# Kernel optimization log

Hardware: AMD Instinct MI355X
Metric: run time of the kernel (lower is better)

## Reference

```python
import jax, jax.numpy as jnp
import numpy as np
import math

NUM_BUCKETS = 32
MAX_DISTANCE = 128
NUM_HEADS = 16
D_MODEL = 1024
HEAD_DIM = D_MODEL // NUM_HEADS


def _relative_position_bucket(relative_position, num_buckets=NUM_BUCKETS, max_distance=MAX_DISTANCE):
    # bidirectional=False path of the original
    rp = -jnp.minimum(relative_position, 0)  # non-negative distances
    max_exact = num_buckets // 2
    is_small = rp < max_exact
    rp_safe = jnp.maximum(rp, 1).astype(jnp.float32)
    rp_if_large = max_exact + (
        jnp.log(rp_safe / max_exact) / math.log(max_distance / max_exact) * (num_buckets - max_exact)
    ).astype(jnp.int32)
    rp_if_large = jnp.minimum(rp_if_large, num_buckets - 1)
    return jnp.where(is_small, rp, rp_if_large)


def relative_bias(rab_weight, q_len, k_len):
    ctx = jnp.arange(q_len)[:, None]
    mem = jnp.arange(k_len)[None, :]
    buckets = _relative_position_bucket(mem - ctx)  # [Q, K]
    vals = rab_weight[buckets]                       # [Q, K, H]
    return jnp.transpose(vals, (2, 0, 1))[None]      # [1, H, Q, K]


def setup_inputs() -> dict:
    key = jax.random.key(0)
    k1, k2, k3, k4 = jax.random.split(key, 4)
    B, S = 4, 2048
    return {
        "v": jax.random.normal(k1, (B, S, D_MODEL), dtype=jnp.float32),
        "k": jax.random.normal(k2, (B, S, D_MODEL), dtype=jnp.float32),
        "q": jax.random.normal(k3, (B, S, D_MODEL), dtype=jnp.float32),
        "rab_weight": jax.random.normal(k4, (NUM_BUCKETS, NUM_HEADS), dtype=jnp.float32),
    }


def reference(v, k, q, rab_weight):
    B, S, _ = q.shape
    def split(x):
        return jnp.transpose(x.reshape(B, S, NUM_HEADS, HEAD_DIM), (0, 2, 1, 3))  # [B,H,S,D]
    qh, kh, vh = split(q), split(k), split(v)
    scores = jnp.einsum("bhqd,bhkd->bhqk", qh, kh)          # [B,H,S,S]
    scores = scores + relative_bias(rab_weight, S, S)        # add relative bias
    av = jnp.einsum("bhqk,bhkd->bhqd", jax.nn.silu(scores), vh)
    return jnp.transpose(av, (0, 2, 1, 3)).reshape(B, S, D_MODEL)
```

## Files before the change

### kernel.cpp

```cpp
#include <hip/hip_runtime.h>

#define NB 4
#define SEQ 2048
#define NH 16
#define HD 64
#define DMODEL 1024

typedef short bf16x8 __attribute__((ext_vector_type(8)));
typedef float f32x16 __attribute__((ext_vector_type(16)));

union FragU {
    bf16x8 v;
    uint2 u2[2];
    unsigned int w[4];
    unsigned short s[8];
};

#if __has_builtin(__builtin_amdgcn_cvt_pk_bf16_f32)
typedef __bf16 v2bf_t __attribute__((ext_vector_type(2)));
__device__ __forceinline__ unsigned int pack_bf16(float lo, float hi) {
    union { v2bf_t h; unsigned int u; } cv;
    cv.h = __builtin_amdgcn_cvt_pk_bf16_f32(lo, hi);
    return cv.u;
}
#else
__device__ __forceinline__ unsigned int pack_bf16(float lo, float hi) {
    unsigned int a = __float_as_uint(lo) + 0x8000u;
    unsigned int b = __float_as_uint(hi) + 0x8000u;
    return __builtin_amdgcn_perm(b, a, 0x07060302);
}
#endif

#define EXP_SCALE 1.44269504f
#define LN2       0.69314718f

__global__ __launch_bounds__(256, 2)
void paa_kernel(const float* __restrict__ Vg, const float* __restrict__ Kg,
                const float* __restrict__ Qg, const float* __restrict__ RW,
                float* __restrict__ Og)
{
    __shared__ __align__(16) unsigned short KsLds[64 * 68];
    __shared__ __align__(16) unsigned short VtLds[64 * 68];
    __shared__ float btab[128];

    const int tid  = threadIdx.x;
    const int lane = tid & 63;
    const int wave = tid >> 6;
    const int half = lane >> 5;
    const int l31  = lane & 31;

    const int bid  = blockIdx.x;
    const int bh   = bid & 63;
    const int qt   = bid >> 6;
    const int b    = bh >> 4;
    const int head = bh & 15;

    const int q0w = qt * 256 + wave * 64;

    if (tid < 128) {
        int rp = tid;
        int bucket;
        if (rp < 16) bucket = rp;
        else {
            int big = 16 + (int)(logf((float)rp * 0.0625f) * 7.6943736f);
            bucket = big < 31 ? big : 31;
        }
        btab[tid] = RW[bucket * NH + head] * EXP_SCALE;
    }

    FragU qf[2][4];
    {
        const float* qbase = Qg + (size_t)(b * SEQ) * DMODEL + head * HD;
        #pragma unroll
        for (int u = 0; u < 2; ++u) {
            const float* qrow = qbase + (size_t)(q0w + u * 32 + l31) * DMODEL;
            #pragma unroll
            for (int kf = 0; kf < 4; ++kf) {
                int dd = kf * 16 + half * 8;
                float4 x0 = *(const float4*)(qrow + dd);
                float4 x1 = *(const float4*)(qrow + dd + 4);
                FragU f;
                f.w[0] = pack_bf16(x0.x * EXP_SCALE, x0.y * EXP_SCALE);
                f.w[1] = pack_bf16(x0.z * EXP_SCALE, x0.w * EXP_SCALE);
                f.w[2] = pack_bf16(x1.x * EXP_SCALE, x1.y * EXP_SCALE);
                f.w[3] = pack_bf16(x1.z * EXP_SCALE, x1.w * EXP_SCALE);
                qf[u][kf] = f;
            }
        }
    }

    f32x16 oacc[2][2];
    #pragma unroll
    for (int u = 0; u < 2; ++u)
        #pragma unroll
        for (int n = 0; n < 2; ++n)
            #pragma unroll
            for (int r = 0; r < 16; ++r) oacc[u][n][r] = 0.0f;

    __syncthreads();
    const float bias_d0  = btab[0];
    const float bias_far = btab[127];

    const int krow0 = tid >> 4;
    const int c4    = tid & 15;
    const int kc4   = tid >> 4;
    const int d4    = tid & 15;

    const float* kthr = Kg + (size_t)(b * SEQ) * DMODEL + head * HD
                      + (size_t)krow0 * DMODEL + c4 * 4;
    const float* vthr = Vg + (size_t)(b * SEQ) * DMODEL + head * HD
                      + (size_t)(kc4 * 4) * DMODEL + d4 * 4;

    float4 kreg[4], vreg[4];
    #pragma unroll
    for (int i = 0; i < 4; ++i) kreg[i] = *(const float4*)(kthr + (size_t)(i * 16) * DMODEL);
    #pragma unroll
    for (int r = 0; r < 4; ++r) vreg[r] = *(const float4*)(vthr + (size_t)r * DMODEL);

    for (int it = 0; it < 32; ++it) {
        const int kcb = it * 64;

        #pragma unroll
        for (int i = 0; i < 4; ++i) {
            uint2 w;
            w.x = pack_bf16(kreg[i].x, kreg[i].y);
            w.y = pack_bf16(kreg[i].z, kreg[i].w);
            *(uint2*)&KsLds[(krow0 + i * 16) * 68 + c4 * 4] = w;
        }
        {
            const float* vr = (const float*)vreg;
            #pragma unroll
            for (int c = 0; c < 4; ++c) {
                uint2 w;
                w.x = pack_bf16(vr[0 * 4 + c], vr[1 * 4 + c]);
                w.y = pack_bf16(vr[2 * 4 + c], vr[3 * 4 + c]);
                *(uint2*)&VtLds[(d4 * 4 + c) * 68 + kc4 * 4] = w;
            }
        }
        __syncthreads();

        if (it < 31) {
            const float* kn = kthr + (size_t)(kcb + 64) * DMODEL;
            const float* vn = vthr + (size_t)(kcb + 64) * DMODEL;
            #pragma unroll
            for (int i = 0; i < 4; ++i) kreg[i] = *(const float4*)(kn + (size_t)(i * 16) * DMODEL);
            #pragma unroll
            for (int r = 0; r < 4; ++r) vreg[r] = *(const float4*)(vn + (size_t)r * DMODEL);
        }

        FragU pf[2][4];
        #pragma unroll
        for (int t = 0; t < 2; ++t) {
            const int kcmin = kcb + t * 32;
            FragU ka[4];
            #pragma unroll
            for (int kf = 0; kf < 4; ++kf) {
                int off = (t * 32 + l31) * 68 + kf * 16 + half * 8;
                ka[kf].u2[0] = *(const uint2*)&KsLds[off];
                ka[kf].u2[1] = *(const uint2*)&KsLds[off + 4];
            }
            f32x16 st[2];
            #pragma unroll
            for (int u = 0; u < 2; ++u) {
                const int qminu = q0w + u * 32;
                if (qminu + 31 - kcmin <= 0) {
                    #pragma unroll
                    for (int r = 0; r < 16; ++r) st[u][r] = bias_d0;
                } else if (qminu - (kcmin + 31) >= 113) {
                    #pragma unroll
                    for (int r = 0; r < 16; ++r) st[u][r] = bias_far;
                } else {
                    const int dql = qminu + l31 - kcmin - 4 * half;
                    #pragma unroll
                    for (int r = 0; r < 16; ++r) {
                        int dv = dql - ((r & 3) + 8 * (r >> 2));
                        dv = dv < 0 ? 0 : (dv > 127 ? 127 : dv);
                        st[u][r] = btab[dv];
                    }
                }
            }
            #pragma unroll
            for (int kf = 0; kf < 4; ++kf)
                #pragma unroll
                for (int u = 0; u < 2; ++u)
                    st[u] = __builtin_amdgcn_mfma_f32_32x32x16_bf16(
                        ka[kf].v, qf[u][kf].v, st[u], 0, 0, 0);

            #pragma unroll
            for (int u = 0; u < 2; ++u) {
                float vals[16];
                #pragma unroll
                for (int r = 0; r < 16; ++r) {
                    float x = st[u][r];
                    float e = __builtin_amdgcn_exp2f(-x);
                    vals[r] = x * __builtin_amdgcn_rcpf(1.0f + e);
                }
                #pragma unroll
                for (int j = 0; j < 4; ++j)
                    pf[u][t * 2].w[j]     = pack_bf16(vals[2 * j], vals[2 * j + 1]);
                #pragma unroll
                for (int j = 0; j < 4; ++j)
                    pf[u][t * 2 + 1].w[j] = pack_bf16(vals[8 + 2 * j], vals[9 + 2 * j]);
            }
        }

        #pragma unroll
        for (int f = 0; f < 4; ++f) {
            #pragma unroll
            for (int n = 0; n < 2; ++n) {
                FragU vf;
                int off = (n * 32 + l31) * 68 + f * 16 + half * 4;
                vf.u2[0] = *(const uint2*)&VtLds[off];
                vf.u2[1] = *(const uint2*)&VtLds[off + 8];
                #pragma unroll
                for (int u = 0; u < 2; ++u)
                    oacc[u][n] = __builtin_amdgcn_mfma_f32_32x32x16_bf16(
                        pf[u][f].v, vf.v, oacc[u][n], 0, 0, 0);
            }
        }
        __syncthreads();
    }

    float* obase = Og + (size_t)(b * SEQ) * DMODEL + head * HD;
    #pragma unroll
    for (int u = 0; u < 2; ++u) {
        #pragma unroll
        for (int r = 0; r < 16; ++r) {
            int q = q0w + u * 32 + (r & 3) + 8 * (r >> 2) + 4 * half;
            float* orow = obase + (size_t)q * DMODEL;
            #pragma unroll
            for (int n = 0; n < 2; ++n)
                orow[n * 32 + l31] = oacc[u][n][r] * LN2;
        }
    }
}

extern "C" void kernel_launch(void* const* d_in, const int* in_sizes, int n_in,
                              void* d_out, int out_size, void* d_ws, size_t ws_size,
                              hipStream_t stream) {
    const float* v  = (const float*)d_in[0];
    const float* k  = (const float*)d_in[1];
    const float* q  = (const float*)d_in[2];
    const float* rw = (const float*)d_in[3];
    float* out = (float*)d_out;
    paa_kernel<<<dim3(512), dim3(256), 0, stream>>>(v, k, q, rw, out);
}
```

Before: 252.5 us.

## Use 512-thread blocks with 32 query rows per wave, dropping register prefetch

Blocks grow from 4 to 8 waves. Each wave now owns 32 query rows instead of 64, so Q fragments, score tiles and output accumulators are halved per thread. The software register prefetch of the next K/V tile is removed: tiles are now loaded from global memory right before being converted and written to LDS. The intent is to cut register pressure and hide memory latency through more resident waves instead of explicit prefetch. In exchange, each wave reads K and V fragments from LDS for half as many MFMAs, and the global loads are no longer overlapped with compute inside a wave.

```diff
diff --git a/kernel.cpp b/kernel.cpp
--- a/kernel.cpp
+++ b/kernel.cpp
@@ -34,7 +34,7 @@
 #define EXP_SCALE 1.44269504f
 #define LN2       0.69314718f
 
-__global__ __launch_bounds__(256, 2)
+__global__ __launch_bounds__(512, 4)
 void paa_kernel(const float* __restrict__ Vg, const float* __restrict__ Kg,
                 const float* __restrict__ Qg, const float* __restrict__ RW,
                 float* __restrict__ Og)
@@ -55,7 +55,7 @@
     const int b    = bh >> 4;
     const int head = bh & 15;
 
-    const int q0w = qt * 256 + wave * 64;
+    const int q0w = qt * 256 + wave * 32;
 
     if (tid < 128) {
         int rp = tid;
@@ -68,87 +68,65 @@
         btab[tid] = RW[bucket * NH + head] * EXP_SCALE;
     }
 
-    FragU qf[2][4];
+    FragU qf[4];
     {
-        const float* qbase = Qg + (size_t)(b * SEQ) * DMODEL + head * HD;
-        #pragma unroll
-        for (int u = 0; u < 2; ++u) {
-            const float* qrow = qbase + (size_t)(q0w + u * 32 + l31) * DMODEL;
-            #pragma unroll
-            for (int kf = 0; kf < 4; ++kf) {
-                int dd = kf * 16 + half * 8;
-                float4 x0 = *(const float4*)(qrow + dd);
-                float4 x1 = *(const float4*)(qrow + dd + 4);
-                FragU f;
-                f.w[0] = pack_bf16(x0.x * EXP_SCALE, x0.y * EXP_SCALE);
-                f.w[1] = pack_bf16(x0.z * EXP_SCALE, x0.w * EXP_SCALE);
-                f.w[2] = pack_bf16(x1.x * EXP_SCALE, x1.y * EXP_SCALE);
-                f.w[3] = pack_bf16(x1.z * EXP_SCALE, x1.w * EXP_SCALE);
-                qf[u][kf] = f;
-            }
-        }
-    }
-
-    f32x16 oacc[2][2];
+        const float* qrow = Qg + (size_t)(b * SEQ + q0w + l31) * DMODEL + head * HD;
+        #pragma unroll
+        for (int kf = 0; kf < 4; ++kf) {
+            int dd = kf * 16 + half * 8;
+            float4 x0 = *(const float4*)(qrow + dd);
+            float4 x1 = *(const float4*)(qrow + dd + 4);
+            FragU f;
+            f.w[0] = pack_bf16(x0.x * EXP_SCALE, x0.y * EXP_SCALE);
+            f.w[1] = pack_bf16(x0.z * EXP_SCALE, x0.w * EXP_SCALE);
+            f.w[2] = pack_bf16(x1.x * EXP_SCALE, x1.y * EXP_SCALE);
+            f.w[3] = pack_bf16(x1.z * EXP_SCALE, x1.w * EXP_SCALE);
+            qf[kf] = f;
+        }
+    }
+
+    f32x16 oacc[2];
     #pragma unroll
-    for (int u = 0; u < 2; ++u)
-        #pragma unroll
-        for (int n = 0; n < 2; ++n)
-            #pragma unroll
-            for (int r = 0; r < 16; ++r) oacc[u][n][r] = 0.0f;
+    for (int n = 0; n < 2; ++n)
+        #pragma unroll
+        for (int r = 0; r < 16; ++r) oacc[n][r] = 0.0f;
 
     __syncthreads();
     const float bias_d0  = btab[0];
     const float bias_far = btab[127];
 
-    const int krow0 = tid >> 4;
-    const int c4    = tid & 15;
-    const int kc4   = tid >> 4;
-    const int d4    = tid & 15;
-
-    const float* kthr = Kg + (size_t)(b * SEQ) * DMODEL + head * HD
-                      + (size_t)krow0 * DMODEL + c4 * 4;
-    const float* vthr = Vg + (size_t)(b * SEQ) * DMODEL + head * HD
-                      + (size_t)(kc4 * 4) * DMODEL + d4 * 4;
-
-    float4 kreg[4], vreg[4];
-    #pragma unroll
-    for (int i = 0; i < 4; ++i) kreg[i] = *(const float4*)(kthr + (size_t)(i * 16) * DMODEL);
-    #pragma unroll
-    for (int r = 0; r < 4; ++r) vreg[r] = *(const float4*)(vthr + (size_t)r * DMODEL);
+    const int krow = tid >> 4;
+    const int c4   = tid & 15;
+    const int kc2  = tid >> 4;
+    const int d4   = tid & 15;
+
+    const float* kbase = Kg + (size_t)(b * SEQ) * DMODEL + head * HD;
+    const float* vbase = Vg + (size_t)(b * SEQ) * DMODEL + head * HD;
 
     for (int it = 0; it < 32; ++it) {
         const int kcb = it * 64;
 
         #pragma unroll
-        for (int i = 0; i < 4; ++i) {
+        for (int i = 0; i < 2; ++i) {
+            int row = krow + i * 32;
+            float4 x = *(const float4*)(kbase + (size_t)(kcb + row) * DMODEL + c4 * 4);
             uint2 w;
-            w.x = pack_bf16(kreg[i].x, kreg[i].y);
-            w.y = pack_bf16(kreg[i].z, kreg[i].w);
-            *(uint2*)&KsLds[(krow0 + i * 16) * 68 + c4 * 4] = w;
+            w.x = pack_bf16(x.x, x.y);
+            w.y = pack_bf16(x.z, x.w);
+            *(uint2*)&KsLds[row * 68 + c4 * 4] = w;
         }
         {
-            const float* vr = (const float*)vreg;
-            #pragma unroll
-            for (int c = 0; c < 4; ++c) {
-                uint2 w;
-                w.x = pack_bf16(vr[0 * 4 + c], vr[1 * 4 + c]);
-                w.y = pack_bf16(vr[2 * 4 + c], vr[3 * 4 + c]);
-                *(uint2*)&VtLds[(d4 * 4 + c) * 68 + kc4 * 4] = w;
-            }
+            const float* vrow = vbase + (size_t)(kcb + kc2 * 2) * DMODEL + d4 * 4;
+            float4 x0 = *(const float4*)(vrow);
+            float4 x1 = *(const float4*)(vrow + DMODEL);
+            *(unsigned int*)&VtLds[(d4 * 4 + 0) * 68 + kc2 * 2] = pack_bf16(x0.x, x1.x);
+            *(unsigned int*)&VtLds[(d4 * 4 + 1) * 68 + kc2 * 2] = pack_bf16(x0.y, x1.y);
+            *(unsigned int*)&VtLds[(d4 * 4 + 2) * 68 + kc2 * 2] = pack_bf16(x0.z, x1.z);
+            *(unsigned int*)&VtLds[(d4 * 4 + 3) * 68 + kc2 * 2] = pack_bf16(x0.w, x1.w);
         }
         __syncthreads();
 
-        if (it < 31) {
-            const float* kn = kthr + (size_t)(kcb + 64) * DMODEL;
-            const float* vn = vthr + (size_t)(kcb + 64) * DMODEL;
-            #pragma unroll
-            for (int i = 0; i < 4; ++i) kreg[i] = *(const float4*)(kn + (size_t)(i * 16) * DMODEL);
-            #pragma unroll
-            for (int r = 0; r < 4; ++r) vreg[r] = *(const float4*)(vn + (size_t)r * DMODEL);
-        }
-
-        FragU pf[2][4];
+        FragU pf[4];
         #pragma unroll
         for (int t = 0; t < 2; ++t) {
             const int kcmin = kcb + t * 32;
@@ -159,49 +137,39 @@
                 ka[kf].u2[0] = *(const uint2*)&KsLds[off];
                 ka[kf].u2[1] = *(const uint2*)&KsLds[off + 4];
             }
-            f32x16 st[2];
-            #pragma unroll
-            for (int u = 0; u < 2; ++u) {
-                const int qminu = q0w + u * 32;
-                if (qminu + 31 - kcmin <= 0) {
-                    #pragma unroll
-                    for (int r = 0; r < 16; ++r) st[u][r] = bias_d0;
-                } else if (qminu - (kcmin + 31) >= 113) {
-                    #pragma unroll
-                    for (int r = 0; r < 16; ++r) st[u][r] = bias_far;
-                } else {
-                    const int dql = qminu + l31 - kcmin - 4 * half;
-                    #pragma unroll
-                    for (int r = 0; r < 16; ++r) {
-                        int dv = dql - ((r & 3) + 8 * (r >> 2));
-                        dv = dv < 0 ? 0 : (dv > 127 ? 127 : dv);
-                        st[u][r] = btab[dv];
-                    }
-                }
-            }
-            #pragma unroll
-            for (int kf = 0; kf < 4; ++kf)
+            f32x16 st;
+            if (q0w + 31 - kcmin <= 0) {
                 #pragma unroll
-                for (int u = 0; u < 2; ++u)
-                    st[u] = __builtin_amdgcn_mfma_f32_32x32x16_bf16(
-                        ka[kf].v, qf[u][kf].v, st[u], 0, 0, 0);
-
-            #pragma unroll
-            for (int u = 0; u < 2; ++u) {
-                float vals[16];
+                for (int r = 0; r < 16; ++r) st[r] = bias_d0;
+            } else if (q0w - (kcmin + 31) >= 113) {
+                #pragma unroll
+                for (int r = 0; r < 16; ++r) st[r] = bias_far;
+            } else {
+                const int dql = q0w + l31 - kcmin - 4 * half;
                 #pragma unroll
                 for (int r = 0; r < 16; ++r) {
-                    float x = st[u][r];
-                    float e = __builtin_amdgcn_exp2f(-x);
-                    vals[r] = x * __builtin_amdgcn_rcpf(1.0f + e);
+                    int dv = dql - ((r & 3) + 8 * (r >> 2));
+                    dv = dv < 0 ? 0 : (dv > 127 ? 127 : dv);
+                    st[r] = btab[dv];
                 }
-                #pragma unroll
-                for (int j = 0; j < 4; ++j)
-                    pf[u][t * 2].w[j]     = pack_bf16(vals[2 * j], vals[2 * j + 1]);
-                #pragma unroll
-                for (int j = 0; j < 4; ++j)
-                    pf[u][t * 2 + 1].w[j] = pack_bf16(vals[8 + 2 * j], vals[9 + 2 * j]);
-            }
+            }
+            #pragma unroll
+            for (int kf = 0; kf < 4; ++kf)
+                st = __builtin_amdgcn_mfma_f32_32x32x16_bf16(ka[kf].v, qf[kf].v, st, 0, 0, 0);
+
+            float vals[16];
+            #pragma unroll
+            for (int r = 0; r < 16; ++r) {
+                float x = st[r];
+                float e = __builtin_amdgcn_exp2f(-x);
+                vals[r] = x * __builtin_amdgcn_rcpf(1.0f + e);
+            }
+            #pragma unroll
+            for (int j = 0; j < 4; ++j)
+                pf[t * 2].w[j]     = pack_bf16(vals[2 * j], vals[2 * j + 1]);
+            #pragma unroll
+            for (int j = 0; j < 4; ++j)
+                pf[t * 2 + 1].w[j] = pack_bf16(vals[8 + 2 * j], vals[9 + 2 * j]);
         }
 
         #pragma unroll
@@ -212,10 +180,7 @@
                 int off = (n * 32 + l31) * 68 + f * 16 + half * 4;
                 vf.u2[0] = *(const uint2*)&VtLds[off];
                 vf.u2[1] = *(const uint2*)&VtLds[off + 8];
-                #pragma unroll
-                for (int u = 0; u < 2; ++u)
-                    oacc[u][n] = __builtin_amdgcn_mfma_f32_32x32x16_bf16(
-                        pf[u][f].v, vf.v, oacc[u][n], 0, 0, 0);
+                oacc[n] = __builtin_amdgcn_mfma_f32_32x32x16_bf16(pf[f].v, vf.v, oacc[n], 0, 0, 0);
             }
         }
         __syncthreads();
@@ -223,15 +188,12 @@
 
     float* obase = Og + (size_t)(b * SEQ) * DMODEL + head * HD;
     #pragma unroll
-    for (int u = 0; u < 2; ++u) {
-        #pragma unroll
-        for (int r = 0; r < 16; ++r) {
-            int q = q0w + u * 32 + (r & 3) + 8 * (r >> 2) + 4 * half;
-            float* orow = obase + (size_t)q * DMODEL;
-            #pragma unroll
-            for (int n = 0; n < 2; ++n)
-                orow[n * 32 + l31] = oacc[u][n][r] * LN2;
-        }
+    for (int r = 0; r < 16; ++r) {
+        int q = q0w + (r & 3) + 8 * (r >> 2) + 4 * half;
+        float* orow = obase + (size_t)q * DMODEL;
+        #pragma unroll
+        for (int n = 0; n < 2; ++n)
+            orow[n * 32 + l31] = oacc[n][r] * LN2;
     }
 }
 
@@ -243,5 +205,5 @@
     const float* q  = (const float*)d_in[2];
     const float* rw = (const float*)d_in[3];
     float* out = (float*)d_out;
-    paa_kernel<<<dim3(512), dim3(256), 0, stream>>>(v, k, q, rw, out);
-}
+    paa_kernel<<<dim3(512), dim3(512), 0, stream>>>(v, k, q, rw, out);
+}
```

Result: faster. 220.4 us (-12.7%).
